# Optimization experiments

Measured on AMD Instinct MI355X. Metric: run time of the kernel, lower is better.

The kernel has to match this reference:

```python
import jax, jax.numpy as jnp
import numpy as np

DIM = 1024
KV_DIM = 768
NUM_HEADS = 16
HEAD_DIM = DIM // NUM_HEADS
EPS = 1e-6


def _rms_norm(h, g):
    var = jnp.mean(h * h, axis=-1, keepdims=True)
    return h * jax.lax.rsqrt(var + EPS) * g


def _rotate_half(t):
    t1, t2 = jnp.split(t, 2, axis=-1)
    return jnp.concatenate((-t2, t1), axis=-1)


def _apply_rope(t, cos, sin):
    # t: [B, L, H, D]; cos/sin: [B, L, D] -> broadcast over heads (unsqueeze_dim=2)
    cos = cos[:, :, None, :]
    sin = sin[:, :, None, :]
    return t * cos + _rotate_half(t) * sin


def setup_inputs() -> dict:
    key = jax.random.key(0)
    ks = jax.random.split(key, 16)
    B, Lq, Lkv = 2, 4096, 1024
    inp = {
        "x": jax.random.normal(ks[0], (B, Lq, DIM), jnp.float32),
        "y": jax.random.normal(ks[1], (B, Lkv, KV_DIM), jnp.float32),
        "x_cos": jax.random.normal(ks[2], (B, Lq, HEAD_DIM), jnp.float32),
        "x_sin": jax.random.normal(ks[3], (B, Lq, HEAD_DIM), jnp.float32),
        "y_cos": jax.random.normal(ks[4], (B, Lkv, HEAD_DIM), jnp.float32),
        "y_sin": jax.random.normal(ks[5], (B, Lkv, HEAD_DIM), jnp.float32),
        # Linear params stored as [in, out] (apply as h @ W + b)
        "Wq": jax.random.normal(ks[6], (DIM, DIM), jnp.float32) * 0.02,
        "bq": jnp.zeros((DIM,), jnp.float32),
        "Wk": jax.random.normal(ks[7], (KV_DIM, DIM), jnp.float32) * 0.02,
        "bk": jnp.zeros((DIM,), jnp.float32),
        "Wv": jax.random.normal(ks[8], (KV_DIM, DIM), jnp.float32) * 0.02,
        "bv": jnp.zeros((DIM,), jnp.float32),
        "Wo": jax.random.normal(ks[9], (DIM, DIM), jnp.float32) * 0.02,
        "bo": jnp.zeros((DIM,), jnp.float32),
        "gq": jnp.ones((DIM,), jnp.float32),   # RMSNorm weight for q
        "gk": jnp.ones((DIM,), jnp.float32),   # RMSNorm weight for k
    }
    return inp


def reference(x, y, x_cos, x_sin, y_cos, y_sin,
              Wq, bq, Wk, bk, Wv, bv, Wo, bo, gq, gk):
    B, Lq, _ = x.shape
    _, Lkv, _ = y.shape
    q = _rms_norm(x @ Wq + bq, gq)              # [B, Lq, DIM]
    k = _rms_norm(y @ Wk + bk, gk)              # [B, Lkv, DIM]
    v = y @ Wv + bv                              # [B, Lkv, DIM]

    q = q.reshape(B, Lq, NUM_HEADS, HEAD_DIM)
    k = k.reshape(B, Lkv, NUM_HEADS, HEAD_DIM)
    v = v.reshape(B, Lkv, NUM_HEADS, HEAD_DIM)

    q = _apply_rope(q, x_cos, x_sin)
    k = _apply_rope(k, y_cos, y_sin)

    scale = HEAD_DIM ** -0.5
    scores = jnp.einsum("blhd,bmhd->bhlm", q, k) * scale   # [B, H, Lq, Lkv]
    probs = jax.nn.softmax(scores, axis=-1)
    out = jnp.einsum("bhlm,bmhd->blhd", probs, v)           # [B, Lq, H, D]
    out = out.reshape(B, Lq, DIM)
    return out @ Wo + bo
```

## Files before the change

kernel.cpp:

```cpp
#include <hip/hip_runtime.h>

typedef __bf16 bf16;
typedef __bf16 bf16x4 __attribute__((ext_vector_type(4)));
typedef __bf16 bf16x8 __attribute__((ext_vector_type(8)));
typedef float  f32x4  __attribute__((ext_vector_type(4)));
typedef float  f32x16 __attribute__((ext_vector_type(16)));
typedef unsigned u32x4 __attribute__((ext_vector_type(4)));

#define NH   16
#define HD   64
#define DQ   1024
#define DKV  768
#define LQ   4096
#define LKV  1024
#define NB   2

__device__ __forceinline__ f32x4 mfma16(bf16x8 a, bf16x8 b, f32x4 c) {
    return __builtin_amdgcn_mfma_f32_16x16x32_bf16(a, b, c, 0, 0, 0);
}
__device__ __forceinline__ f32x16 mfma32(bf16x8 a, bf16x8 b, f32x16 c) {
    return __builtin_amdgcn_mfma_f32_32x32x16_bf16(a, b, c, 0, 0, 0);
}

__device__ __forceinline__ void plswap(unsigned &a, unsigned &b) {
#if __has_builtin(__builtin_amdgcn_permlane32_swap)
    auto r = __builtin_amdgcn_permlane32_swap(a, b, false, false);
    a = (unsigned)r[0]; b = (unsigned)r[1];
#else
    asm volatile("v_permlane32_swap_b32 %0, %1" : "+v"(a), "+v"(b));
#endif
}

__device__ __forceinline__ float xhalf_max(float v) {
    unsigned t = __builtin_bit_cast(unsigned, v), u = t;
    plswap(t, u);
    return fmaxf(__builtin_bit_cast(float, t), __builtin_bit_cast(float, u));
}
__device__ __forceinline__ float xhalf_add(float v) {
    unsigned t = __builtin_bit_cast(unsigned, v), u = t;
    plswap(t, u);
    return __builtin_bit_cast(float, t) + __builtin_bit_cast(float, u);
}

#define F3(a, b, c) fmaxf(fmaxf((a), (b)), (c))
__device__ __forceinline__ float vmax32(const f32x16& A, const f32x16& B) {
    float t0 = F3(A[0],  A[1],  A[2]);
    float t1 = F3(A[3],  A[4],  A[5]);
    float t2 = F3(A[6],  A[7],  A[8]);
    float t3 = F3(A[9],  A[10], A[11]);
    float t4 = F3(A[12], A[13], A[14]);
    float t5 = F3(A[15], B[0],  B[1]);
    float t6 = F3(B[2],  B[3],  B[4]);
    float t7 = F3(B[5],  B[6],  B[7]);
    float t8 = F3(B[8],  B[9],  B[10]);
    float t9 = F3(B[11], B[12], B[13]);
    float ta = fmaxf(B[14], B[15]);
    float u0 = F3(t0, t1, t2);
    float u1 = F3(t3, t4, t5);
    float u2 = F3(t6, t7, t8);
    float u3 = fmaxf(t9, ta);
    return fmaxf(F3(u0, u1, u2), u3);
}
__device__ __forceinline__ float vsum16(const f32x16& S) {
    float a = (S[0]  + S[1])  + (S[2]  + S[3]);
    float b = (S[4]  + S[5])  + (S[6]  + S[7]);
    float c = (S[8]  + S[9])  + (S[10] + S[11]);
    float d = (S[12] + S[13]) + (S[14] + S[15]);
    return (a + b) + (c + d);
}

__device__ __forceinline__ void cvtpk16(const f32x16& S, unsigned dw[8]) {
#pragma unroll
    for (int g = 0; g < 4; g++)
#pragma unroll
        for (int hh = 0; hh < 2; hh++) {
            unsigned d_;
            asm("v_cvt_pk_bf16_f32 %0, %1, %2"
                : "=v"(d_) : "v"(S[4 * g + 2 * hh]), "v"(S[4 * g + 2 * hh + 1]));
            dw[g * 2 + hh] = d_;
        }
}

#define GLDS16(g, l) __builtin_amdgcn_global_load_lds(                      \
    (const __attribute__((address_space(1))) void*)(g),                     \
    (__attribute__((address_space(3))) void*)(l), 16, 0, 0)

__global__ __launch_bounds__(256) void prep(
        const float* __restrict__ Wq, const float* __restrict__ Wk,
        const float* __restrict__ Wv, const float* __restrict__ Wo,
        bf16* __restrict__ Wq_t, bf16* __restrict__ Wk_t,
        bf16* __restrict__ Wv_t, bf16* __restrict__ Wo_t,
        const float* __restrict__ x, const float* __restrict__ y,
        bf16* __restrict__ xb, bf16* __restrict__ yb,
        int nx8, int ntot8) {
    if (blockIdx.z < 4) {
        __shared__ float tile[32][33];
        const float* in; bf16* out; int K;
        switch (blockIdx.z) {
            case 0:  in = Wq; out = Wq_t; K = DQ;  break;
            case 1:  in = Wk; out = Wk_t; K = DKV; break;
            case 2:  in = Wv; out = Wv_t; K = DKV; break;
            default: in = Wo; out = Wo_t; K = DQ;  break;
        }
        int n0 = blockIdx.x * 32, k0 = blockIdx.y * 32;
        if (k0 >= K) return;
        int tx = threadIdx.x, ty = threadIdx.y;
        for (int yy = 0; yy < 32; yy += 8)
            tile[ty + yy][tx] = in[(size_t)(k0 + ty + yy) * DQ + n0 + tx];
        __syncthreads();
        for (int yy = 0; yy < 32; yy += 8)
            out[(size_t)(n0 + ty + yy) * K + k0 + tx] = (bf16)tile[tx][ty + yy];
    } else {
        int tid = threadIdx.y * 32 + threadIdx.x;
        int flat = (blockIdx.y * 32 + blockIdx.x) * 256 + tid;
        for (int i = flat; i < ntot8; i += 32 * 32 * 256) {
            const float* in; bf16* out; int j;
            if (i < nx8) { in = x; out = xb; j = i; }
            else         { in = y; out = yb; j = i - nx8; }
            float4 a0 = ((const float4*)in)[(size_t)j * 2];
            float4 a1 = ((const float4*)in)[(size_t)j * 2 + 1];
            bf16x8 v = {(bf16)a0.x, (bf16)a0.y, (bf16)a0.z, (bf16)a0.w,
                        (bf16)a1.x, (bf16)a1.y, (bf16)a1.z, (bf16)a1.w};
            ((bf16x8*)out)[j] = v;
        }
    }
}

template <int MODE>
__device__ __forceinline__ void gemm_body(bf16* __restrict__ sm,
                                          const bf16* __restrict__ A,
                                          const bf16* __restrict__ Bt,
                                          const float* __restrict__ bias,
                                          void* __restrict__ Cv,
                                          int N, int K, int m0, int n0) {
    bf16* As = sm;
    bf16* Bs = sm + 2 * 4096;
    int tid  = threadIdx.x;
    int lane = tid & 63, w = tid >> 6;
    int quad = lane >> 4, l15 = lane & 15;
    int wm = (w >> 1) * 64, wn = (w & 1) * 64;
    int srow = tid >> 2;
    int scol = ((tid & 3) ^ (srow & 3)) * 8;
    const bf16* Ag = &A [(size_t)(m0 + srow) * K + scol];
    const bf16* Bg = &Bt[(size_t)(n0 + srow) * K + scol];
    int woff = w * 512;
    int fcol = ((quad ^ (l15 & 3)) * 8);

    f32x4 acc[4][4] = {};
    int nit = K >> 5;

#define STAGE(buf, kk) do {                                              \
        int k0_ = (kk) << 5;                                             \
        bf16* a_ = As + (buf) * 4096 + woff;                             \
        bf16* b_ = Bs + (buf) * 4096 + woff;                             \
        GLDS16(Ag + k0_,                  a_);                           \
        GLDS16(Ag + (size_t)64 * K + k0_, a_ + 2048);                    \
        GLDS16(Bg + k0_,                  b_);                           \
        GLDS16(Bg + (size_t)64 * K + k0_, b_ + 2048);                    \
    } while (0)

    STAGE(0, 0);
    __syncthreads();

    for (int t = 0; t < nit; t++) {
        int cur = t & 1;
        if (t + 1 < nit) STAGE(cur ^ 1, t + 1);
        const bf16* Ac = As + cur * 4096;
        const bf16* Bc = Bs + cur * 4096;
        bf16x8 af[4], bfr[4];
#pragma unroll
        for (int i = 0; i < 4; i++)
            af[i] = *(const bf16x8*)&Ac[(wm + i * 16 + l15) * 32 + fcol];
#pragma unroll
        for (int j = 0; j < 4; j++)
            bfr[j] = *(const bf16x8*)&Bc[(wn + j * 16 + l15) * 32 + fcol];
#pragma unroll
        for (int i = 0; i < 4; i++)
#pragma unroll
            for (int j = 0; j < 4; j++)
                acc[i][j] = mfma16(af[i], bfr[j], acc[i][j]);
        __syncthreads();
    }
#undef STAGE

    bf16*  Cb = (bf16*)Cv;
    float* Cf = (float*)Cv;
#pragma unroll
    for (int i = 0; i < 4; i++)
#pragma unroll
        for (int j = 0; j < 4; j++) {
            int col = n0 + wn + j * 16 + l15;
            float bcol = bias[col];
            if (MODE == 1) {
                int rowb = m0 + wm + i * 16 + quad * 4;
                int bb = rowb >> 10, kv = rowb & 1023;
                int h = col >> 6, d = col & 63;
                bf16x4 val = {(bf16)(acc[i][j][0] + bcol), (bf16)(acc[i][j][1] + bcol),
                              (bf16)(acc[i][j][2] + bcol), (bf16)(acc[i][j][3] + bcol)};
                *(bf16x4*)&Cb[(((size_t)(bb * NH + h) * HD) + d) * LKV + kv] = val;
            } else {
#pragma unroll
                for (int r = 0; r < 4; r++) {
                    int row = m0 + wm + i * 16 + quad * 4 + r;
                    float v = acc[i][j][r] + bcol;
                    if (MODE == 2) Cf[(size_t)row * N + col] = v;
                    else           Cb[(size_t)row * N + col] = (bf16)v;
                }
            }
        }
}

__global__ __launch_bounds__(256, 3) void gemm_qkv(
        const bf16* xb, const bf16* Wq_t, const float* bq, bf16* qbuf,
        const bf16* yb, const bf16* Wk_t, const float* bk, bf16* kbuf,
        const bf16* Wv_t, const float* bv, bf16* vT) {
    __shared__ bf16 sm[4 * 4096];
    int lin  = blockIdx.y * 8 + blockIdx.x;
    int work = (lin & 7) * 96 + (lin >> 3);
    int xt = work & 7, yt = work >> 3;
    if (yt < 64)      gemm_body<0>(sm, xb, Wq_t, bq, qbuf, DQ, DQ,  yt * 128,        xt * 128);
    else if (yt < 80) gemm_body<0>(sm, yb, Wk_t, bk, kbuf, DQ, DKV, (yt - 64) * 128, xt * 128);
    else              gemm_body<1>(sm, yb, Wv_t, bv, vT,   DQ, DKV, (yt - 80) * 128, xt * 128);
}
__global__ __launch_bounds__(256, 3) void gemm_o(const bf16* A, const bf16* Bt,
                                                 const float* bias, void* Cv) {
    __shared__ bf16 sm[4 * 4096];
    int lin  = blockIdx.y * 8 + blockIdx.x;
    int work = (lin & 7) * 64 + (lin >> 3);
    int xt = work & 7, yt = work >> 3;
    gemm_body<2>(sm, A, Bt, bias, Cv, DQ, DQ, yt * 128, xt * 128);
}

__global__ __launch_bounds__(256) void rmsnorm_rope3(bf16* __restrict__ qb,
                                                     bf16* __restrict__ kb,
                                                     const float* __restrict__ gq,
                                                     const float* __restrict__ gk,
                                                     const float* __restrict__ xc,
                                                     const float* __restrict__ xs,
                                                     const float* __restrict__ yc,
                                                     const float* __restrict__ ys) {
    int w = threadIdx.x >> 6, lane = threadIdx.x & 63;
    int row = blockIdx.x * 4 + w;
    bf16* t; const float *g, *cs, *sn;
    if (row < NB * LQ) {
        t = qb + (size_t)row * DQ; g = gq;
        cs = xc + (size_t)row * HD; sn = xs + (size_t)row * HD;
    } else {
        int r2 = row - NB * LQ;
        t = kb + (size_t)r2 * DQ; g = gk;
        cs = yc + (size_t)r2 * HD; sn = ys + (size_t)r2 * HD;
    }
    int c0 = lane * 16;
    bf16x8 a0 = *(const bf16x8*)&t[c0];
    bf16x8 a1 = *(const bf16x8*)&t[c0 + 8];
    float vv[16], ss = 0.f;
#pragma unroll
    for (int j = 0; j < 8; j++) { vv[j] = (float)a0[j]; vv[8 + j] = (float)a1[j]; }
#pragma unroll
    for (int j = 0; j < 16; j++) ss += vv[j] * vv[j];
#pragma unroll
    for (int off = 32; off >= 1; off >>= 1) ss += __shfl_xor(ss, off, 64);
    float rms = rsqrtf(ss * (1.0f / 1024.0f) + 1e-6f);
    float nv[16];
#pragma unroll
    for (int j = 0; j < 16; j++) nv[j] = vv[j] * rms * g[c0 + j];
    int d0 = (lane & 3) * 16;
    float sgn = (lane & 2) ? 1.f : -1.f;
    bf16x8 o0, o1;
#pragma unroll
    for (int j = 0; j < 16; j++) {
        float pv = __shfl_xor(nv[j], 2, 64);
        float r = nv[j] * cs[d0 + j] + sgn * pv * sn[d0 + j];
        if (j < 8) o0[j] = (bf16)r; else o1[j - 8] = (bf16)r;
    }
    *(bf16x8*)&t[c0]     = o0;
    *(bf16x8*)&t[c0 + 8] = o1;
}

__global__ __launch_bounds__(256, 4) void attn_kern(const bf16* __restrict__ q,
                                                    const bf16* __restrict__ k,
                                                    const bf16* __restrict__ vT,
                                                    bf16* __restrict__ o) {
    __shared__ bf16 Ks[2][64][64];
    __shared__ bf16 Vs[2][64][64];
    int tid = threadIdx.x, w = tid >> 6, lane = tid & 63;
    int l31 = lane & 31, hi = lane >> 5;
    int lin  = blockIdx.x + (blockIdx.y << 5) + (blockIdx.z << 9);
    int work = (lin & 7) * 128 + (lin >> 3);
    int qt = work & 31, h = (work >> 5) & 15, b = work >> 9;
    int qrow = qt * 128 + w * 32 + l31;
    int sw8 = (l31 & 7) << 3;

    bf16x8 qf[4];
    {
        const bf16* qg = &q[((size_t)(b * LQ) + qrow) * DQ + h * HD + hi * 8];
#pragma unroll
        for (int kc = 0; kc < 4; kc++) {
            bf16x8 tq = *(const bf16x8*)(qg + kc * 16);
#pragma unroll
            for (int e = 0; e < 8; e++) tq[e] = (bf16)((float)tq[e] * 0.125f);
            qf[kc] = tq;
        }
    }

    int rb = w * 16;
    int srow = rb + (lane >> 3);
    int sl = (lane & 7) ^ (srow & 7);
    const bf16* kg0 = &k[((size_t)(b * LKV) + srow) * DQ + h * HD + sl * 8];
    const bf16* vg0 = &vT[(((size_t)(b * NH + h) * HD) + srow) * LKV + sl * 8];

    GLDS16(kg0,                   &Ks[0][rb][0]);
    GLDS16(kg0 + (size_t)8 * DQ,  &Ks[0][rb + 8][0]);
    GLDS16(vg0,                   &Vs[0][rb][0]);
    GLDS16(vg0 + (size_t)8 * LKV, &Vs[0][rb + 8][0]);
    __syncthreads();

    f32x16 O0 = {}, O1 = {};
    float m_run = -1e30f, l_run = 0.f;

    for (int i = 0; i < 16; i++) {
        int cur = i & 1;
        if (i < 15) {
            int nxt = cur ^ 1;
            size_t ko = (size_t)(i + 1) * 64 * DQ;
            int    vo = (i + 1) * 64;
            GLDS16(kg0 + ko,                   &Ks[nxt][rb][0]);
            GLDS16(kg0 + ko + (size_t)8 * DQ,  &Ks[nxt][rb + 8][0]);
            GLDS16(vg0 + vo,                   &Vs[nxt][rb][0]);
            GLDS16(vg0 + vo + (size_t)8 * LKV, &Vs[nxt][rb + 8][0]);
        }
        f32x16 S0 = {}, S1 = {};
        __builtin_amdgcn_s_setprio(1);
#pragma unroll
        for (int kc = 0; kc < 4; kc++) {
            bf16x8 kf0 = *(const bf16x8*)&Ks[cur][l31][(kc * 16 + hi * 8) ^ sw8];
            bf16x8 kf1 = *(const bf16x8*)&Ks[cur][32 + l31][(kc * 16 + hi * 8) ^ sw8];
            S0 = mfma32(kf0, qf[kc], S0);
            S1 = mfma32(kf1, qf[kc], S1);
        }
        __builtin_amdgcn_s_setprio(0);
        float pmax = vmax32(S0, S1);
        if (!__all(pmax - m_run <= 8.f)) {
            float pm2 = xhalf_max(pmax);
            float mn = fmaxf(m_run, pm2);
            float alpha = __expf(m_run - mn);
            m_run = mn; l_run *= alpha;
#pragma unroll
            for (int r = 0; r < 16; r++) { O0[r] *= alpha; O1[r] *= alpha; }
        }
#pragma unroll
        for (int r = 0; r < 16; r++) S0[r] = __expf(S0[r] - m_run);
#pragma unroll
        for (int r = 0; r < 16; r++) S1[r] = __expf(S1[r] - m_run);
        float rs = vsum16(S0) + vsum16(S1);
        l_run += xhalf_add(rs);
        unsigned dw0[8], dw1[8];
        cvtpk16(S0, dw0);
        {
            unsigned a0 = dw0[0], b0 = dw0[2], a1 = dw0[1], b1 = dw0[3];
            unsigned c0 = dw0[4], e0 = dw0[6], c1 = dw0[5], e1 = dw0[7];
            plswap(a0, b0); plswap(a1, b1);
            plswap(c0, e0); plswap(c1, e1);
            u32x4 pw0 = {a0, a1, b0, b1};
            u32x4 pw1 = {c0, c1, e0, e1};
            bf16x8 pba = __builtin_bit_cast(bf16x8, pw0);
            bf16x8 pbb = __builtin_bit_cast(bf16x8, pw1);
            int vc0 = (hi * 8) ^ sw8;
            int vc1 = (16 + hi * 8) ^ sw8;
            bf16x8 vfa0 = *(const bf16x8*)&Vs[cur][l31][vc0];
            bf16x8 vfa1 = *(const bf16x8*)&Vs[cur][32 + l31][vc0];
            bf16x8 vfb0 = *(const bf16x8*)&Vs[cur][l31][vc1];
            bf16x8 vfb1 = *(const bf16x8*)&Vs[cur][32 + l31][vc1];
            __builtin_amdgcn_s_setprio(1);
            O0 = mfma32(vfa0, pba, O0);
            O1 = mfma32(vfa1, pba, O1);
            O0 = mfma32(vfb0, pbb, O0);
            O1 = mfma32(vfb1, pbb, O1);
            __builtin_amdgcn_s_setprio(0);
        }
        cvtpk16(S1, dw1);
        {
            unsigned a0 = dw1[0], b0 = dw1[2], a1 = dw1[1], b1 = dw1[3];
            unsigned c0 = dw1[4], e0 = dw1[6], c1 = dw1[5], e1 = dw1[7];
            plswap(a0, b0); plswap(a1, b1);
            plswap(c0, e0); plswap(c1, e1);
            u32x4 pw0 = {a0, a1, b0, b1};
            u32x4 pw1 = {c0, c1, e0, e1};
            bf16x8 pba = __builtin_bit_cast(bf16x8, pw0);
            bf16x8 pbb = __builtin_bit_cast(bf16x8, pw1);
            int vc0 = (32 + hi * 8) ^ sw8;
            int vc1 = (48 + hi * 8) ^ sw8;
            bf16x8 vfa0 = *(const bf16x8*)&Vs[cur][l31][vc0];
            bf16x8 vfa1 = *(const bf16x8*)&Vs[cur][32 + l31][vc0];
            bf16x8 vfb0 = *(const bf16x8*)&Vs[cur][l31][vc1];
            bf16x8 vfb1 = *(const bf16x8*)&Vs[cur][32 + l31][vc1];
            __builtin_amdgcn_s_setprio(1);
            O0 = mfma32(vfa0, pba, O0);
            O1 = mfma32(vfa1, pba, O1);
            O0 = mfma32(vfb0, pbb, O0);
            O1 = mfma32(vfb1, pbb, O1);
            __builtin_amdgcn_s_setprio(0);
        }
        if (i < 15) __syncthreads();
    }

    float inv = 1.0f / l_run;
    size_t ob = ((size_t)(b * LQ) + qrow) * DQ + h * HD;
#pragma unroll
    for (int td = 0; td < 2; td++) {
        const f32x16& O = td ? O1 : O0;
#pragma unroll
        for (int g = 0; g < 4; g++) {
            bf16x4 ov = {(bf16)(O[4 * g + 0] * inv), (bf16)(O[4 * g + 1] * inv),
                         (bf16)(O[4 * g + 2] * inv), (bf16)(O[4 * g + 3] * inv)};
            *(bf16x4*)&o[ob + td * 32 + g * 8 + hi * 4] = ov;
        }
    }
}

extern "C" void kernel_launch(void* const* d_in, const int* in_sizes, int n_in,
                              void* d_out, int out_size, void* d_ws, size_t ws_size,
                              hipStream_t stream) {
    const float* x     = (const float*)d_in[0];
    const float* y     = (const float*)d_in[1];
    const float* x_cos = (const float*)d_in[2];
    const float* x_sin = (const float*)d_in[3];
    const float* y_cos = (const float*)d_in[4];
    const float* y_sin = (const float*)d_in[5];
    const float* Wq    = (const float*)d_in[6];
    const float* bq    = (const float*)d_in[7];
    const float* Wk    = (const float*)d_in[8];
    const float* bk    = (const float*)d_in[9];
    const float* Wv    = (const float*)d_in[10];
    const float* bv    = (const float*)d_in[11];
    const float* Wo    = (const float*)d_in[12];
    const float* bo    = (const float*)d_in[13];
    const float* gq    = (const float*)d_in[14];
    const float* gk    = (const float*)d_in[15];

    char* ws = (char*)d_ws;
    bf16* Wq_t = (bf16*)ws;  ws += (size_t)DQ * DQ * 2;
    bf16* Wk_t = (bf16*)ws;  ws += (size_t)DQ * DKV * 2;
    bf16* Wv_t = (bf16*)ws;  ws += (size_t)DQ * DKV * 2;
    bf16* Wo_t = (bf16*)ws;  ws += (size_t)DQ * DQ * 2;
    bf16* qbuf = (bf16*)ws;  ws += (size_t)NB * LQ * DQ * 2;
    bf16* kbuf = (bf16*)ws;  ws += (size_t)NB * LKV * DQ * 2;
    bf16* vT   = (bf16*)ws;  ws += (size_t)NB * NH * HD * LKV * 2;
    bf16* aout = (bf16*)ws;  ws += (size_t)NB * LQ * DQ * 2;
    bf16* yb   = (bf16*)ws;  ws += (size_t)NB * LKV * DKV * 2;
    bf16* xb   = aout;

    int nx8 = NB * LQ * DQ / 8, ny8 = NB * LKV * DKV / 8;
    prep<<<dim3(32, 32, 5), dim3(32, 8), 0, stream>>>(
        Wq, Wk, Wv, Wo, Wq_t, Wk_t, Wv_t, Wo_t,
        x, y, xb, yb, nx8, nx8 + ny8);

    gemm_qkv<<<dim3(8, 96), 256, 0, stream>>>(
        xb, Wq_t, bq, qbuf, yb, Wk_t, bk, kbuf, Wv_t, bv, vT);

    rmsnorm_rope3<<<NB * (LQ + LKV) / 4, 256, 0, stream>>>(
        qbuf, kbuf, gq, gk, x_cos, x_sin, y_cos, y_sin);

    attn_kern<<<dim3(LQ / 128, NH, NB), 256, 0, stream>>>(qbuf, kbuf, vT, aout);

    gemm_o<<<dim3(DQ / 128, NB * LQ / 128), 256, 0, stream>>>(aout, Wo_t, bo, d_out);
}
```

Baseline: 241.4 us.

## Load V fragments directly from global into registers instead of staging through LDS

Removes the double-buffered LDS staging of V and has each lane read its V^T fragments straight from global memory at the start of each KV tile, feeding them directly into the MFMAs. The row-sum cross-half reduction is also deferred from every iteration to once after the loop. This cuts LDS traffic and footprint (possibly raising occupancy) and removes per-iteration shuffles. The cost is that V global loads are now issued per wave without prefetching a tile ahead, so their latency may be exposed, and each of the four waves redundantly loads the same V data.

After: 295.5 us. 22.4% more time.

```diff
diff --git a/kernel.cpp b/kernel.cpp
--- a/kernel.cpp
+++ b/kernel.cpp
@@ -282,7 +282,6 @@
                                                     const bf16* __restrict__ vT,
                                                     bf16* __restrict__ o) {
     __shared__ bf16 Ks[2][64][64];
-    __shared__ bf16 Vs[2][64][64];
     int tid = threadIdx.x, w = tid >> 6, lane = tid & 63;
     int l31 = lane & 31, hi = lane >> 5;
     int lin  = blockIdx.x + (blockIdx.y << 5) + (blockIdx.z << 9);
@@ -307,27 +306,32 @@
     int srow = rb + (lane >> 3);
     int sl = (lane & 7) ^ (srow & 7);
     const bf16* kg0 = &k[((size_t)(b * LKV) + srow) * DQ + h * HD + sl * 8];
-    const bf16* vg0 = &vT[(((size_t)(b * NH + h) * HD) + srow) * LKV + sl * 8];
-
-    GLDS16(kg0,                   &Ks[0][rb][0]);
-    GLDS16(kg0 + (size_t)8 * DQ,  &Ks[0][rb + 8][0]);
-    GLDS16(vg0,                   &Vs[0][rb][0]);
-    GLDS16(vg0 + (size_t)8 * LKV, &Vs[0][rb + 8][0]);
+    const bf16* vb0 = &vT[(((size_t)(b * NH + h) * HD) + l31) * LKV + hi * 8];
+    const bf16* vb1 = &vT[(((size_t)(b * NH + h) * HD) + 32 + l31) * LKV + hi * 8];
+
+    GLDS16(kg0,                  &Ks[0][rb][0]);
+    GLDS16(kg0 + (size_t)8 * DQ, &Ks[0][rb + 8][0]);
     __syncthreads();
 
     f32x16 O0 = {}, O1 = {};
-    float m_run = -1e30f, l_run = 0.f;
+    float m_run = -1e30f, l_acc = 0.f;
 
     for (int i = 0; i < 16; i++) {
         int cur = i & 1;
+        int vo = i * 64;
+        bf16x8 v00 = *(const bf16x8*)(vb0 + vo);
+        bf16x8 v01 = *(const bf16x8*)(vb0 + vo + 16);
+        bf16x8 v02 = *(const bf16x8*)(vb0 + vo + 32);
+        bf16x8 v03 = *(const bf16x8*)(vb0 + vo + 48);
+        bf16x8 v10 = *(const bf16x8*)(vb1 + vo);
+        bf16x8 v11 = *(const bf16x8*)(vb1 + vo + 16);
+        bf16x8 v12 = *(const bf16x8*)(vb1 + vo + 32);
+        bf16x8 v13 = *(const bf16x8*)(vb1 + vo + 48);
         if (i < 15) {
             int nxt = cur ^ 1;
             size_t ko = (size_t)(i + 1) * 64 * DQ;
-            int    vo = (i + 1) * 64;
-            GLDS16(kg0 + ko,                   &Ks[nxt][rb][0]);
-            GLDS16(kg0 + ko + (size_t)8 * DQ,  &Ks[nxt][rb + 8][0]);
-            GLDS16(vg0 + vo,                   &Vs[nxt][rb][0]);
-            GLDS16(vg0 + vo + (size_t)8 * LKV, &Vs[nxt][rb + 8][0]);
+            GLDS16(kg0 + ko,                  &Ks[nxt][rb][0]);
+            GLDS16(kg0 + ko + (size_t)8 * DQ, &Ks[nxt][rb + 8][0]);
         }
         f32x16 S0 = {}, S1 = {};
         __builtin_amdgcn_s_setprio(1);
@@ -344,7 +348,7 @@
             float pm2 = xhalf_max(pmax);
             float mn = fmaxf(m_run, pm2);
             float alpha = __expf(m_run - mn);
-            m_run = mn; l_run *= alpha;
+            m_run = mn; l_acc *= alpha;
 #pragma unroll
             for (int r = 0; r < 16; r++) { O0[r] *= alpha; O1[r] *= alpha; }
         }
@@ -352,8 +356,7 @@
         for (int r = 0; r < 16; r++) S0[r] = __expf(S0[r] - m_run);
 #pragma unroll
         for (int r = 0; r < 16; r++) S1[r] = __expf(S1[r] - m_run);
-        float rs = vsum16(S0) + vsum16(S1);
-        l_run += xhalf_add(rs);
+        l_acc += vsum16(S0) + vsum16(S1);
         unsigned dw0[8], dw1[8];
         cvtpk16(S0, dw0);
         {
@@ -365,17 +368,11 @@
             u32x4 pw1 = {c0, c1, e0, e1};
             bf16x8 pba = __builtin_bit_cast(bf16x8, pw0);
             bf16x8 pbb = __builtin_bit_cast(bf16x8, pw1);
-            int vc0 = (hi * 8) ^ sw8;
-            int vc1 = (16 + hi * 8) ^ sw8;
-            bf16x8 vfa0 = *(const bf16x8*)&Vs[cur][l31][vc0];
-            bf16x8 vfa1 = *(const bf16x8*)&Vs[cur][32 + l31][vc0];
-            bf16x8 vfb0 = *(const bf16x8*)&Vs[cur][l31][vc1];
-            bf16x8 vfb1 = *(const bf16x8*)&Vs[cur][32 + l31][vc1];
             __builtin_amdgcn_s_setprio(1);
-            O0 = mfma32(vfa0, pba, O0);
-            O1 = mfma32(vfa1, pba, O1);
-            O0 = mfma32(vfb0, pbb, O0);
-            O1 = mfma32(vfb1, pbb, O1);
+            O0 = mfma32(v00, pba, O0);
+            O1 = mfma32(v10, pba, O1);
+            O0 = mfma32(v01, pbb, O0);
+            O1 = mfma32(v11, pbb, O1);
             __builtin_amdgcn_s_setprio(0);
         }
         cvtpk16(S1, dw1);
@@ -388,22 +385,17 @@
             u32x4 pw1 = {c0, c1, e0, e1};
             bf16x8 pba = __builtin_bit_cast(bf16x8, pw0);
             bf16x8 pbb = __builtin_bit_cast(bf16x8, pw1);
-            int vc0 = (32 + hi * 8) ^ sw8;
-            int vc1 = (48 + hi * 8) ^ sw8;
-            bf16x8 vfa0 = *(const bf16x8*)&Vs[cur][l31][vc0];
-            bf16x8 vfa1 = *(const bf16x8*)&Vs[cur][32 + l31][vc0];
-            bf16x8 vfb0 = *(const bf16x8*)&Vs[cur][l31][vc1];
-            bf16x8 vfb1 = *(const bf16x8*)&Vs[cur][32 + l31][vc1];
             __builtin_amdgcn_s_setprio(1);
-            O0 = mfma32(vfa0, pba, O0);
-            O1 = mfma32(vfa1, pba, O1);
-            O0 = mfma32(vfb0, pbb, O0);
-            O1 = mfma32(vfb1, pbb, O1);
+            O0 = mfma32(v02, pba, O0);
+            O1 = mfma32(v12, pba, O1);
+            O0 = mfma32(v03, pbb, O0);
+            O1 = mfma32(v13, pbb, O1);
             __builtin_amdgcn_s_setprio(0);
         }
         if (i < 15) __syncthreads();
     }
 
+    float l_run = xhalf_add(l_acc);
     float inv = 1.0f / l_run;
     size_t ob = ((size_t)(b * LQ) + qrow) * DQ + h * HD;
 #pragma unroll
```
